# Optimization experiments

Measured on AMD Instinct MI355X. Metric: run time of the kernel, lower is better.

Reference implementation:

```python
import jax, jax.numpy as jnp
import numpy as np

NUM_ITER = 5  # num_iterations
M, N, B = 972, 1944, 8  # check_matrix_row, check_matrix_column, unit_batch_size
ROW_DEG = 8  # check-node degree of the sparse parity matrix


def setup_inputs() -> dict:
    key = jax.random.key(0)
    # sparse binary parity-check matrix H (constant Tanner graph)
    rng = np.random.default_rng(0)
    H = np.zeros((M, N), np.float32)
    for i in range(M):
        H[i, rng.choice(N, ROW_DEG, replace=False)] = 1.0
    soft_input = 2.0 * jax.random.normal(key, (B, N), dtype=jnp.float32)  # channel LLRs
    check_weight = jnp.array([-1.07], dtype=jnp.float32)  # NMS init constant
    return {"soft_input": soft_input, "H": jnp.asarray(H), "check_weight": check_weight}


def _bp_iteration(cv, soft_input, H, check_weight):
    # ---- compute_vc (NMS: bit weight == 1.0) ----
    total = jnp.sum(cv, axis=1) + soft_input              # [B, N]
    vc = total[:, None, :] * H - cv                       # [B, M, N]
    # ---- compute_cv (min-sum branch) ----
    back = jnp.where(H == 0, -1e30 - 1.0, 0.0)[None]      # mask non-edges
    a = jnp.clip(jnp.abs(vc), 0.0, 1e30)
    dec = -a + back
    top2, _ = jax.lax.top_k(dec, 2)                       # [B, M, 2]
    min1 = (-top2[..., 0])[:, :, None] * H                # row min broadcast on edges
    min2 = (-top2[..., 1])[:, :, None] * H                # row second-min
    result = jnp.where(a > min1, min1, min2)              # exclude-self min
    sign_info = (1.0 - H)[None] + vc
    s = jnp.sign(sign_info)
    tot_sign = jnp.prod(s, axis=2)[:, :, None] * H
    result_sign = tot_sign * s                            # exclude-self sign product
    w = jax.nn.softplus(check_weight)                     # scalar NMS factor
    cv_new = result * jax.lax.stop_gradient(result_sign) * w
    return cv_new


def reference(soft_input, H, check_weight):
    Bn, n = soft_input.shape
    m = H.shape[0]
    cv0 = jnp.zeros((Bn, m, n), dtype=soft_input.dtype)

    def body(cv, _):
        return _bp_iteration(cv, soft_input, H, check_weight), None

    cv, _ = jax.lax.scan(body, cv0, None, length=NUM_ITER)
    # marginalize
    soft_output = jnp.sum(cv, axis=1) + soft_input
    return soft_output
```

## Files before the change

kernel.cpp:

```cpp
#include <hip/hip_runtime.h>
#include <math.h>

#define MM 972
#define NN 1944
#define BB 8
#define RD 8
#define NITER 5
#define MAXD 16
#define POISON 0xAAAAAAAAu

__device__ __forceinline__ void emit_edge(int m, int n, int* cnt,
                                          unsigned* __restrict__ col_cnt,
                                          int2* __restrict__ row_edges) {
    int j = atomicAdd(cnt, 1);
    unsigned k = atomicAdd(&col_cnt[n], 1u) - POISON;
    if (k > MAXD - 1u) k = MAXD - 1u;
    int kk = (int)k;
    int phys = (((((kk >> 2) + n + (n >> 1)) & 3) << 2) | (kk & 3));
    row_edges[m * RD + j] = make_int2(n, n * MAXD + phys);
}

__global__ __launch_bounds__(256) void build_adj(const float* __restrict__ H,
                                                 unsigned* __restrict__ col_cnt,
                                                 int2* __restrict__ row_edges) {
    const int m = blockIdx.x;
    __shared__ int cnt;
    if (threadIdx.x == 0) cnt = 0;
    __syncthreads();
    const float4* H4 = (const float4*)(H + (size_t)m * NN);
    for (int q = threadIdx.x; q < NN / 4; q += blockDim.x) {
        float4 h = H4[q];
        int n = 4 * q;
        if (h.x != 0.0f) emit_edge(m, n + 0, &cnt, col_cnt, row_edges);
        if (h.y != 0.0f) emit_edge(m, n + 1, &cnt, col_cnt, row_edges);
        if (h.z != 0.0f) emit_edge(m, n + 2, &cnt, col_cnt, row_edges);
        if (h.w != 0.0f) emit_edge(m, n + 3, &cnt, col_cnt, row_edges);
    }
}

__global__ __launch_bounds__(1024, 1) void decode(const float* __restrict__ soft,
                                                  const float* __restrict__ cwp,
                                                  const unsigned* __restrict__ col_cnt,
                                                  const int2* __restrict__ row_edges,
                                                  float* __restrict__ out) {
    __shared__ __align__(16) float cvc[NN * MAXD];
    __shared__ float tot[NN];

    const int b = blockIdx.x;
    const int t = threadIdx.x;
    const float* soft_b = soft + b * NN;

    int rc[RD], rs[RD];
    float cv[RD];
    if (t < MM) {
        const int2* rep = row_edges + t * RD;
#pragma unroll
        for (int j = 0; j < RD; ++j) {
            int2 e = rep[j];
            rc[j] = e.x;
            rs[j] = e.y;
            cv[j] = 0.0f;
        }
    }

    const int n0 = t;
    const int n1 = t + 1024;
    const bool has1 = (n1 < NN);
    const int n1c = has1 ? n1 : 0;
    const float s0 = soft_b[n0];
    const float s1 = has1 ? soft_b[n1] : 0.0f;
    const int g0 = (n0 + (n0 >> 1)) & 3;
    const int g1 = (n1c + (n1c >> 1)) & 3;
    const unsigned d0 = col_cnt[n0] - POISON;
    const unsigned d1 = has1 ? (col_cnt[n1] - POISON) : 0u;
    const int C0 = ((int)min(d0, (unsigned)MAXD) + 3) >> 2;
    const int C1 = ((int)min(d1, (unsigned)MAXD) + 3) >> 2;

    const float w = log1pf(expf(cwp[0]));

    float4* cv4 = (float4*)cvc;
#pragma unroll
    for (int i = 0; i < 8; ++i) {
        int idx = t + i * 1024;
        if (idx < NN * MAXD / 4) cv4[idx] = make_float4(0.f, 0.f, 0.f, 0.f);
    }
    tot[n0] = s0;
    if (has1) tot[n1] = s1;
    __syncthreads();

    for (int it = 0; it < NITER; ++it) {
        if (t < MM) {
            float v[RD];
            float m1 = 3.0e38f, m2 = 3.0e38f, p = 1.0f;
#pragma unroll
            for (int j = 0; j < RD; ++j) {
                float vv = tot[rc[j]] - cv[j];
                v[j] = vv;
                float a = fabsf(vv);
                float s = (vv > 0.0f) ? 1.0f : ((vv < 0.0f) ? -1.0f : 0.0f);
                p *= s;
                if (a < m1) { m2 = m1; m1 = a; }
                else if (a < m2) { m2 = a; }
            }
            const float pw = p * w;
#pragma unroll
            for (int j = 0; j < RD; ++j) {
                float a = fabsf(v[j]);
                float mag = (a > m1) ? m1 : m2;
                float s = (v[j] > 0.0f) ? 1.0f : ((v[j] < 0.0f) ? -1.0f : 0.0f);
                float nc = mag * s * pw;
                cv[j] = nc;
                cvc[rs[j]] = nc;
            }
        }
        __syncthreads();

        float a0 = 0.0f, a1 = 0.0f;
#pragma unroll
        for (int i = 0; i < 4; ++i) {
            if (i < C0) {
                float4 q = cv4[n0 * 4 + ((i + g0) & 3)];
                a0 += (q.x + q.y) + (q.z + q.w);
            }
            if (i < C1) {
                float4 q = cv4[n1c * 4 + ((i + g1) & 3)];
                a1 += (q.x + q.y) + (q.z + q.w);
            }
        }
        const float t0 = s0 + a0;
        const float t1 = s1 + a1;
        if (it == NITER - 1) {
            out[b * NN + n0] = t0;
            if (has1) out[b * NN + n1] = t1;
        } else {
            tot[n0] = t0;
            if (has1) tot[n1] = t1;
            __syncthreads();
        }
    }
}

extern "C" void kernel_launch(void* const* d_in, const int* in_sizes, int n_in,
                              void* d_out, int out_size, void* d_ws, size_t ws_size,
                              hipStream_t stream) {
    const float* soft = (const float*)d_in[0];
    const float* H    = (const float*)d_in[1];
    const float* cw   = (const float*)d_in[2];
    float* out = (float*)d_out;

    unsigned* col_cnt = (unsigned*)d_ws;
    int2* row_edges   = (int2*)(col_cnt + NN);

    build_adj<<<MM, 256, 0, stream>>>(H, col_cnt, row_edges);
    decode<<<BB, 1024, 0, stream>>>(soft, cw, col_cnt, row_edges, out);
}
```

Measured before the change: 75.38 us.

## Grid-stride adjacency build, pack edge index, bitwise min-sum sign/magnitude

build_adj becomes a grid-stride scan over H with 256 blocks instead of one block per row. It skips all-zero float4 chunks and uses a global per-row atomic counter that relies on the workspace poison value. Edge records shrink from int2 to one int, with the column recovered as slot>>4. The check-node update now finds minima on raw float bits and gets the sign product by XOR, replacing sign multiplies with bit ops. This relies on zero-handling subtleties: a zero-valued message forces the output to zero via m1==0, though a -0.0 input may be treated differently than sign()==0.

```diff
diff --git a/kernel.cpp b/kernel.cpp
--- a/kernel.cpp
+++ b/kernel.cpp
@@ -9,39 +9,39 @@
 #define MAXD 16
 #define POISON 0xAAAAAAAAu
 
-__device__ __forceinline__ void emit_edge(int m, int n, int* cnt,
-                                          unsigned* __restrict__ col_cnt,
-                                          int2* __restrict__ row_edges) {
-    int j = atomicAdd(cnt, 1);
-    unsigned k = atomicAdd(&col_cnt[n], 1u) - POISON;
-    if (k > MAXD - 1u) k = MAXD - 1u;
-    int kk = (int)k;
-    int phys = (((((kk >> 2) + n + (n >> 1)) & 3) << 2) | (kk & 3));
-    row_edges[m * RD + j] = make_int2(n, n * MAXD + phys);
-}
-
 __global__ __launch_bounds__(256) void build_adj(const float* __restrict__ H,
                                                  unsigned* __restrict__ col_cnt,
-                                                 int2* __restrict__ row_edges) {
-    const int m = blockIdx.x;
-    __shared__ int cnt;
-    if (threadIdx.x == 0) cnt = 0;
-    __syncthreads();
-    const float4* H4 = (const float4*)(H + (size_t)m * NN);
-    for (int q = threadIdx.x; q < NN / 4; q += blockDim.x) {
+                                                 unsigned* __restrict__ row_cnt,
+                                                 int* __restrict__ row_edges) {
+    const float4* H4 = (const float4*)H;
+    const int total4 = MM * NN / 4;
+    const int stride = gridDim.x * blockDim.x;
+    for (int q = blockIdx.x * blockDim.x + threadIdx.x; q < total4; q += stride) {
         float4 h = H4[q];
-        int n = 4 * q;
-        if (h.x != 0.0f) emit_edge(m, n + 0, &cnt, col_cnt, row_edges);
-        if (h.y != 0.0f) emit_edge(m, n + 1, &cnt, col_cnt, row_edges);
-        if (h.z != 0.0f) emit_edge(m, n + 2, &cnt, col_cnt, row_edges);
-        if (h.w != 0.0f) emit_edge(m, n + 3, &cnt, col_cnt, row_edges);
+        if (h.x == 0.0f && h.y == 0.0f && h.z == 0.0f && h.w == 0.0f) continue;
+        int idx = 4 * q;
+        int m = idx / NN;
+        int nb = idx - m * NN;
+        float v[4] = {h.x, h.y, h.z, h.w};
+#pragma unroll
+        for (int c = 0; c < 4; ++c) {
+            if (v[c] != 0.0f) {
+                int n = nb + c;
+                unsigned j = atomicAdd(&row_cnt[m], 1u) - POISON;
+                unsigned k = atomicAdd(&col_cnt[n], 1u) - POISON;
+                if (k > MAXD - 1u) k = MAXD - 1u;
+                int kk = (int)k;
+                int phys = (((((kk >> 2) + n + (n >> 1)) & 3) << 2) | (kk & 3));
+                row_edges[m * RD + (int)j] = n * MAXD + phys;
+            }
+        }
     }
 }
 
 __global__ __launch_bounds__(1024, 1) void decode(const float* __restrict__ soft,
                                                   const float* __restrict__ cwp,
                                                   const unsigned* __restrict__ col_cnt,
-                                                  const int2* __restrict__ row_edges,
+                                                  const int* __restrict__ row_edges,
                                                   float* __restrict__ out) {
     __shared__ __align__(16) float cvc[NN * MAXD];
     __shared__ float tot[NN];
@@ -53,12 +53,12 @@
     int rc[RD], rs[RD];
     float cv[RD];
     if (t < MM) {
-        const int2* rep = row_edges + t * RD;
+        const int* rep = row_edges + t * RD;
 #pragma unroll
         for (int j = 0; j < RD; ++j) {
-            int2 e = rep[j];
-            rc[j] = e.x;
-            rs[j] = e.y;
+            int s = rep[j];
+            rs[j] = s;
+            rc[j] = s >> 4;
             cv[j] = 0.0f;
         }
     }
@@ -90,25 +90,27 @@
 
     for (int it = 0; it < NITER; ++it) {
         if (t < MM) {
-            float v[RD];
-            float m1 = 3.0e38f, m2 = 3.0e38f, p = 1.0f;
+            unsigned ab[RD];
+            unsigned sg[RD];
+            unsigned m1 = 0x7f800000u, m2 = 0x7f800000u, sx = 0u;
 #pragma unroll
             for (int j = 0; j < RD; ++j) {
                 float vv = tot[rc[j]] - cv[j];
-                v[j] = vv;
-                float a = fabsf(vv);
-                float s = (vv > 0.0f) ? 1.0f : ((vv < 0.0f) ? -1.0f : 0.0f);
-                p *= s;
+                unsigned u = __float_as_uint(vv);
+                sg[j] = u;
+                sx ^= u;
+                unsigned a = u & 0x7fffffffu;
+                ab[j] = a;
                 if (a < m1) { m2 = m1; m1 = a; }
                 else if (a < m2) { m2 = a; }
             }
-            const float pw = p * w;
+            const float we = (m1 == 0u) ? 0.0f : w;
+            const unsigned sxb = sx & 0x80000000u;
 #pragma unroll
             for (int j = 0; j < RD; ++j) {
-                float a = fabsf(v[j]);
-                float mag = (a > m1) ? m1 : m2;
-                float s = (v[j] > 0.0f) ? 1.0f : ((v[j] < 0.0f) ? -1.0f : 0.0f);
-                float nc = mag * s * pw;
+                unsigned mag = (ab[j] > m1) ? m1 : m2;
+                unsigned sb  = (sg[j] ^ sxb) & 0x80000000u;
+                float nc = __uint_as_float(mag | sb) * we;
                 cv[j] = nc;
                 cvc[rs[j]] = nc;
             }
@@ -149,8 +151,9 @@
     float* out = (float*)d_out;
 
     unsigned* col_cnt = (unsigned*)d_ws;
-    int2* row_edges   = (int2*)(col_cnt + NN);
+    unsigned* row_cnt = col_cnt + NN;
+    int* row_edges    = (int*)(row_cnt + MM);
 
-    build_adj<<<MM, 256, 0, stream>>>(H, col_cnt, row_edges);
+    build_adj<<<256, 256, 0, stream>>>(H, col_cnt, row_cnt, row_edges);
     decode<<<BB, 1024, 0, stream>>>(soft, cw, col_cnt, row_edges, out);
 }
```

New measurement: 79.92 us. 6.0% more time.
